# Performance work log

Measured on AMD Instinct MI355X. Metric: run time of the kernel, lower is better.

The kernel has to match this reference:

```python
import jax, jax.numpy as jnp
import numpy as np

B, IN_DIM, H, L, P = 256, 64, 768, 4, 8
EPS = 1e-5


def _layernorm(h, g, b):
    mu = jnp.mean(h, axis=-1, keepdims=True)
    var = jnp.mean((h - mu) ** 2, axis=-1, keepdims=True)
    return (h - mu) * jax.lax.rsqrt(var + EPS) * g + b


def setup_inputs() -> dict:
    key = jax.random.key(0)
    ks = jax.random.split(key, 20)
    s_in = 1.0 / np.sqrt(IN_DIM)
    s_h = 1.0 / np.sqrt(H)
    return {
        "x": jax.random.normal(ks[0], (B, IN_DIM), jnp.float32),
        "w_in": jax.random.normal(ks[1], (IN_DIM, H), jnp.float32) * s_in,
        "b_in": jnp.zeros((H,), jnp.float32),
        "ln_g": jnp.ones((L, H), jnp.float32),
        "ln_b": jnp.zeros((L, H), jnp.float32),
        "trop_w": jax.random.normal(ks[2], (L, H, H), jnp.float32) * s_h,  # [L, out, in]
        "trop_b": jnp.zeros((L, H), jnp.float32),
        "lf_amax": jax.random.normal(ks[3], (L, H, P), jnp.float32) * 0.5 + 1.0,
        "lf_bmax": jax.random.normal(ks[4], (L, H, P), jnp.float32) * 0.1,
        "lf_amin": jax.random.normal(ks[5], (L, H, P), jnp.float32) * 0.5 + 1.0,
        "lf_bmin": jax.random.normal(ks[6], (L, H, P), jnp.float32) * 0.1,
        "lf_alpha": jnp.zeros((L, H), jnp.float32),
        "gate_w": jax.random.normal(ks[7], (L, H, H), jnp.float32) * 0.02,
        "gate_b": jnp.full((L, H), 2.0, jnp.float32),
        "cls_w": jax.random.normal(ks[8], (L, H, H), jnp.float32) * s_h,
        "cls_b": jnp.zeros((L, H), jnp.float32),
        "out_g": jnp.ones((H,), jnp.float32),
        "out_b": jnp.zeros((H,), jnp.float32),
        "head_w": jax.random.normal(ks[9], (H, 1), jnp.float32) * s_h,
        "head_b": jnp.zeros((1,), jnp.float32),
    }


def reference(x, w_in, b_in, ln_g, ln_b, trop_w, trop_b, lf_amax, lf_bmax,
              lf_amin, lf_bmin, lf_alpha, gate_w, gate_b, cls_w, cls_b,
              out_g, out_b, head_w, head_b):
    h = x @ w_in + b_in  # [B, H]
    for l in range(L):
        res = h
        hn = _layernorm(h, ln_g[l], ln_b[l])
        # Tropical (max-plus) linear: y[b,o] = max_i(hn[b,i] + W[o,i]) + bias[o]
        t = jnp.max(hn[:, None, :] + trop_w[l][None, :, :], axis=-1) + trop_b[l]
        # LF dual activation: blend of convex (max-plus) and concave (min-plus) PWL
        fmax = jnp.max(t[..., None] * lf_amax[l] + lf_bmax[l], axis=-1)  # [B, H]
        fmin = jnp.min(t[..., None] * lf_amin[l] + lf_bmin[l], axis=-1)
        a = jax.nn.sigmoid(lf_alpha[l])
        trop_out = a * fmax + (1.0 - a) * fmin
        class_out = jax.nn.gelu(hn @ cls_w[l] + cls_b[l], approximate=False)
        g = jax.nn.sigmoid(hn @ gate_w[l] + gate_b[l])
        h = res + g * trop_out + (1.0 - g) * class_out
    h = _layernorm(h, out_g, out_b)
    return (h @ head_w + head_b).squeeze(-1)  # [B]
```

## Files before the change

kernel.cpp:

```cpp
#include <hip/hip_runtime.h>
#include <math.h>

#define HDIM 768
#define BDIM 256
#define INDIM 64
#define NLAYERS 4
#define PDIM 8
#define KSPLIT 24
#define KLEN 32
#define CHK 16
#define TR 128
#define TC 64
#define NTROPBLK 576
#define NCGBLK 192
#define NBLK (NTROPBLK + NCGBLK)

typedef short bf16x8 __attribute__((ext_vector_type(8)));
typedef float f32x4 __attribute__((ext_vector_type(4)));

__device__ __forceinline__ float sigmoidf_(float x) { return 1.f / (1.f + expf(-x)); }
__device__ __forceinline__ float geluf_(float x) { return 0.5f * x * (1.f + erff(x * 0.70710678118654752f)); }
__device__ __forceinline__ unsigned short f2bf(float f) {
    unsigned int u = __float_as_uint(f);
    u += 0x7FFFu + ((u >> 16) & 1u);
    return (unsigned short)(u >> 16);
}

__device__ __forceinline__ void gload_lds16(const float* g, float* l) {
    __builtin_amdgcn_global_load_lds((const __attribute__((address_space(1))) void*)g,
                                     (__attribute__((address_space(3))) void*)l, 16, 0, 0);
}

__global__ __launch_bounds__(256) void prep_k(const float* __restrict__ trop_w,
                                              const float* __restrict__ cls_w,
                                              const float* __restrict__ gate_w,
                                              float* __restrict__ twT,
                                              unsigned short* __restrict__ wB)
{
    __shared__ float tile[64][65];
    const int z = blockIdx.z;
    const int a0 = blockIdx.x * 64;
    const int b0 = blockIdx.y * 64;
    const int c = threadIdx.x & 63;
    const int r4 = threadIdx.x >> 6;

    if (z < NLAYERS) {
        const float* s = trop_w + (size_t)z * HDIM * HDIM;
        float* d = twT + (size_t)z * HDIM * HDIM;
#pragma unroll
        for (int it = 0; it < 16; ++it) {
            const int r = it * 4 + r4;
            tile[r][c] = s[(size_t)(a0 + r) * HDIM + b0 + c];
        }
        __syncthreads();
#pragma unroll
        for (int it = 0; it < 16; ++it) {
            const int r = it * 4 + r4;
            d[(size_t)(b0 + r) * HDIM + a0 + c] = tile[c][r];
        }
    } else {
        const int zz = z - NLAYERS;
        const int l = zz >> 1, mat = zz & 1;
        const float* s = (mat ? gate_w : cls_w) + (size_t)l * HDIM * HDIM;
        unsigned short* d = wB + (size_t)zz * HDIM * HDIM;
#pragma unroll
        for (int it = 0; it < 16; ++it) {
            const int r = it * 4 + r4;
            tile[r][c] = s[(size_t)(b0 + r) * HDIM + a0 + c];
        }
        __syncthreads();
#pragma unroll
        for (int it = 0; it < 16; ++it) {
            const int r = it * 4 + r4;
            d[(size_t)(a0 + r) * HDIM + b0 + c] = f2bf(tile[c][r]);
        }
    }
}

__global__ __launch_bounds__(256) void input_ln_k(
    const float* __restrict__ x, const float* __restrict__ w_in,
    const float* __restrict__ b_in,
    const float* __restrict__ lng, const float* __restrict__ lnb,
    float* __restrict__ h, float* __restrict__ hnT, unsigned short* __restrict__ hnB)
{
    const int b = blockIdx.x;
    const int t = threadIdx.x;
    __shared__ float xs[INDIM];
    __shared__ float rbuf[8];
    if (t < INDIM) xs[t] = x[b * INDIM + t];
    __syncthreads();

    float acc0 = b_in[t], acc1 = b_in[t + 256], acc2 = b_in[t + 512];
#pragma unroll 8
    for (int i = 0; i < INDIM; ++i) {
        const float xv = xs[i];
        acc0 = fmaf(xv, w_in[i * HDIM + t], acc0);
        acc1 = fmaf(xv, w_in[i * HDIM + t + 256], acc1);
        acc2 = fmaf(xv, w_in[i * HDIM + t + 512], acc2);
    }
    h[(size_t)b * HDIM + t] = acc0;
    h[(size_t)b * HDIM + t + 256] = acc1;
    h[(size_t)b * HDIM + t + 512] = acc2;

    float s = acc0 + acc1 + acc2;
    float q = acc0 * acc0 + acc1 * acc1 + acc2 * acc2;
#pragma unroll
    for (int off = 32; off > 0; off >>= 1) { s += __shfl_down(s, off); q += __shfl_down(q, off); }
    const int wid = t >> 6, lane = t & 63;
    if (lane == 0) { rbuf[wid] = s; rbuf[4 + wid] = q; }
    __syncthreads();
    s = rbuf[0] + rbuf[1] + rbuf[2] + rbuf[3];
    q = rbuf[4] + rbuf[5] + rbuf[6] + rbuf[7];
    const float mu = s * (1.f / HDIM);
    const float var = q * (1.f / HDIM) - mu * mu;
    const float rsig = rsqrtf(var + 1e-5f);

#pragma unroll
    for (int qq = 0; qq < 3; ++qq) {
        const int o = t + qq * 256;
        const float av = (qq == 0) ? acc0 : (qq == 1) ? acc1 : acc2;
        const float v = (av - mu) * rsig * lng[o] + lnb[o];
        hnT[(size_t)o * BDIM + b] = v;
        hnB[(size_t)b * HDIM + o] = f2bf(v);
    }
}

__global__ __launch_bounds__(256, 2) void layer_mm_k(
    const float* __restrict__ hnT,
    const float* __restrict__ twT,
    const unsigned short* __restrict__ hnB,
    const unsigned short* __restrict__ wB,
    float* __restrict__ p_trop, float* __restrict__ p_cls, float* __restrict__ p_gate)
{
    __shared__ float hn_s[2][CHK][TR];
    __shared__ float wt_s[2][CHK][TC];

    const int bx = blockIdx.x;
    const int tid = threadIdx.x;
    const int wave = tid >> 6, lane = tid & 63;

    if (bx < NTROPBLK) {
        const int sp = bx % 24;
        const int slot = bx / 24;
        const int col0 = (sp % 12) * TC;
        const int row0 = (sp / 12) * TR;
        const int k0 = slot * KLEN;

        const int tx = tid & 15, ty = tid >> 4;
        const int r0 = ty * 8, c0 = tx * 4;

        const int hk = lane >> 5;
        const int hcol = (lane & 31) * 4;
        const int wr = lane >> 4;
        const int wcol = (lane & 15) * 4;

        float t_acc[8][4];
#pragma unroll
        for (int i = 0; i < 8; ++i)
#pragma unroll
            for (int j = 0; j < 4; ++j) t_acc[i][j] = -1e30f;

        #define STAGE_T(buf, kb)                                                                   \
        {                                                                                          \
            gload_lds16(hnT + (size_t)((kb) + 4 * wave + hk) * BDIM + row0 + hcol,                 \
                        &hn_s[buf][4 * wave][0]);                                                  \
            gload_lds16(hnT + (size_t)((kb) + 4 * wave + 2 + hk) * BDIM + row0 + hcol,             \
                        &hn_s[buf][4 * wave + 2][0]);                                              \
            gload_lds16(twT + (size_t)((kb) + 4 * wave + wr) * HDIM + col0 + wcol,                 \
                        &wt_s[buf][4 * wave][0]);                                                  \
        }

        STAGE_T(0, k0);
        __builtin_amdgcn_s_waitcnt(0);
        __syncthreads();

        for (int c = 0; c < KLEN / CHK; ++c) {
            const int buf = c & 1;
            if (c + 1 < KLEN / CHK) STAGE_T(1 - buf, k0 + (c + 1) * CHK);
#pragma unroll
            for (int k = 0; k < CHK; ++k) {
                const float4 h0 = *(const float4*)&hn_s[buf][k][r0];
                const float4 h1 = *(const float4*)&hn_s[buf][k][r0 + 4];
                const float4 wt = *(const float4*)&wt_s[buf][k][c0];
                const float hf[8] = {h0.x, h0.y, h0.z, h0.w, h1.x, h1.y, h1.z, h1.w};
                const float wtf[4] = {wt.x, wt.y, wt.z, wt.w};
#pragma unroll
                for (int i = 0; i < 8; ++i)
#pragma unroll
                    for (int j = 0; j < 4; ++j)
                        t_acc[i][j] = fmaxf(t_acc[i][j], hf[i] + wtf[j]);
            }
            __builtin_amdgcn_s_waitcnt(0);
            __syncthreads();
        }
        #undef STAGE_T

        const size_t base = (size_t)slot * BDIM * HDIM;
#pragma unroll
        for (int i = 0; i < 8; ++i) {
            const size_t off = base + (size_t)(row0 + r0 + i) * HDIM + col0 + c0;
            *(float4*)(p_trop + off) = make_float4(t_acc[i][0], t_acc[i][1], t_acc[i][2], t_acc[i][3]);
        }
    } else {
        const int cb = bx - NTROPBLK;
        const int mat = cb & 1;
        const int nt = (cb >> 1) % 24;
        const int mt = cb / 48;
        const int m0 = mt * 64 + wave * 16;
        const int n0 = nt * 32;
        const int lm = lane & 15, q = lane >> 4;

        const unsigned short* wmat = wB + (size_t)mat * HDIM * HDIM;
        float* pout = mat ? p_gate : p_cls;

        f32x4 acc[2];
        acc[0] = (f32x4){0.f, 0.f, 0.f, 0.f};
        acc[1] = (f32x4){0.f, 0.f, 0.f, 0.f};

        const unsigned short* aptr = hnB + (size_t)(m0 + lm) * HDIM + q * 8;
        const unsigned short* b0 = wmat + (size_t)(n0 + lm) * HDIM + q * 8;
        const unsigned short* b1 = b0 + (size_t)16 * HDIM;

#pragma unroll 4
        for (int k0 = 0; k0 < HDIM; k0 += 32) {
            const bf16x8 a  = *(const bf16x8*)(aptr + k0);
            const bf16x8 v0 = *(const bf16x8*)(b0 + k0);
            const bf16x8 v1 = *(const bf16x8*)(b1 + k0);
            acc[0] = __builtin_amdgcn_mfma_f32_16x16x32_bf16(a, v0, acc[0], 0, 0, 0);
            acc[1] = __builtin_amdgcn_mfma_f32_16x16x32_bf16(a, v1, acc[1], 0, 0, 0);
        }

#pragma unroll
        for (int nn = 0; nn < 2; ++nn)
#pragma unroll
            for (int r = 0; r < 4; ++r)
                pout[(size_t)(m0 + q * 4 + r) * HDIM + n0 + nn * 16 + lm] = acc[nn][r];
    }
}

__global__ __launch_bounds__(768) void combine_k(
    const float* __restrict__ p_trop, const float* __restrict__ p_cls, const float* __restrict__ p_gate,
    const float* __restrict__ trop_b,
    const float* __restrict__ amax, const float* __restrict__ bmax,
    const float* __restrict__ amin, const float* __restrict__ bmin,
    const float* __restrict__ alpha,
    const float* __restrict__ gate_b, const float* __restrict__ cls_b,
    float* __restrict__ h,
    const float* __restrict__ lng, const float* __restrict__ lnb,
    float* __restrict__ hnT, unsigned short* __restrict__ hnB,
    const float* __restrict__ head_w, const float* __restrict__ head_b,
    float* __restrict__ out, const int is_last)
{
    const int b = blockIdx.x;
    const int o = threadIdx.x;
    __shared__ float rbuf[12], qbuf[12];

    const size_t base = (size_t)b * HDIM + o;
    float tm = -1e30f;
#pragma unroll
    for (int k = 0; k < KSPLIT; ++k)
        tm = fmaxf(tm, p_trop[(size_t)k * BDIM * HDIM + base]);
    const float cs = p_cls[base];
    const float gs = p_gate[base];

    const float tv = tm + trop_b[o];
    float fmx = -1e30f, fmn = 1e30f;
#pragma unroll
    for (int p = 0; p < PDIM; ++p) {
        fmx = fmaxf(fmx, fmaf(tv, amax[o * PDIM + p], bmax[o * PDIM + p]));
        fmn = fminf(fmn, fmaf(tv, amin[o * PDIM + p], bmin[o * PDIM + p]));
    }
    const float a = sigmoidf_(alpha[o]);
    const float trop_out = a * fmx + (1.f - a) * fmn;
    const float cls_out = geluf_(cs + cls_b[o]);
    const float g = sigmoidf_(gs + gate_b[o]);
    const float val = h[base] + g * trop_out + (1.f - g) * cls_out;
    h[base] = val;

    float s = val, q = val * val;
#pragma unroll
    for (int off = 32; off > 0; off >>= 1) { s += __shfl_down(s, off); q += __shfl_down(q, off); }
    const int wid = o >> 6, lane = o & 63;
    if (lane == 0) { rbuf[wid] = s; qbuf[wid] = q; }
    __syncthreads();
    s = 0.f; q = 0.f;
#pragma unroll
    for (int w = 0; w < 12; ++w) { s += rbuf[w]; q += qbuf[w]; }
    const float mu = s * (1.f / HDIM);
    const float var = q * (1.f / HDIM) - mu * mu;
    const float rsig = rsqrtf(var + 1e-5f);
    const float ln_v = (val - mu) * rsig * lng[o] + lnb[o];

    if (!is_last) {
        hnT[(size_t)o * BDIM + b] = ln_v;
        hnB[base] = f2bf(ln_v);
    } else {
        float part = ln_v * head_w[o];
#pragma unroll
        for (int off = 32; off > 0; off >>= 1) part += __shfl_down(part, off);
        __syncthreads();
        if (lane == 0) rbuf[wid] = part;
        __syncthreads();
        if (o == 0) {
            float r = head_b[0];
#pragma unroll
            for (int w = 0; w < 12; ++w) r += rbuf[w];
            out[b] = r;
        }
    }
}

extern "C" void kernel_launch(void* const* d_in, const int* in_sizes, int n_in,
                              void* d_out, int out_size, void* d_ws, size_t ws_size,
                              hipStream_t stream)
{
    const float* x       = (const float*)d_in[0];
    const float* w_in    = (const float*)d_in[1];
    const float* b_in    = (const float*)d_in[2];
    const float* ln_g    = (const float*)d_in[3];
    const float* ln_b    = (const float*)d_in[4];
    const float* trop_w  = (const float*)d_in[5];
    const float* trop_b  = (const float*)d_in[6];
    const float* lf_amax = (const float*)d_in[7];
    const float* lf_bmax = (const float*)d_in[8];
    const float* lf_amin = (const float*)d_in[9];
    const float* lf_bmin = (const float*)d_in[10];
    const float* lf_alpha= (const float*)d_in[11];
    const float* gate_w  = (const float*)d_in[12];
    const float* gate_b  = (const float*)d_in[13];
    const float* cls_w   = (const float*)d_in[14];
    const float* cls_b   = (const float*)d_in[15];
    const float* out_g   = (const float*)d_in[16];
    const float* out_b   = (const float*)d_in[17];
    const float* head_w  = (const float*)d_in[18];
    const float* head_b  = (const float*)d_in[19];
    float* out = (float*)d_out;

    const size_t NBH = (size_t)BDIM * HDIM;
    const size_t WSZ = (size_t)HDIM * HDIM;
    float* ws = (float*)d_ws;
    float* h      = ws;
    float* hnT    = ws + NBH;
    float* twT    = ws + 2 * NBH;
    float* p_trop = twT + (size_t)NLAYERS * WSZ;
    float* p_cls  = p_trop + (size_t)KSPLIT * NBH;
    float* p_gate = p_cls + NBH;
    unsigned short* hnB = (unsigned short*)(p_gate + NBH);
    unsigned short* wB  = hnB + NBH;

    prep_k<<<dim3(12, 12, 12), 256, 0, stream>>>(trop_w, cls_w, gate_w, twT, wB);
    input_ln_k<<<BDIM, 256, 0, stream>>>(x, w_in, b_in, ln_g, ln_b, h, hnT, hnB);

    for (int l = 0; l < NLAYERS; ++l) {
        layer_mm_k<<<NBLK, 256, 0, stream>>>(
            hnT, twT + (size_t)l * WSZ,
            hnB, wB + (size_t)(2 * l) * WSZ,
            p_trop, p_cls, p_gate);

        const int is_last = (l == NLAYERS - 1);
        combine_k<<<BDIM, 768, 0, stream>>>(
            p_trop, p_cls, p_gate,
            trop_b + (size_t)l * HDIM,
            lf_amax + (size_t)l * HDIM * PDIM, lf_bmax + (size_t)l * HDIM * PDIM,
            lf_amin + (size_t)l * HDIM * PDIM, lf_bmin + (size_t)l * HDIM * PDIM,
            lf_alpha + (size_t)l * HDIM,
            gate_b + (size_t)l * HDIM, cls_b + (size_t)l * HDIM,
            h,
            is_last ? out_g : ln_g + (size_t)(l + 1) * HDIM,
            is_last ? out_b : ln_b + (size_t)(l + 1) * HDIM,
            hnT, hnB, head_w, head_b, out, is_last);
    }
}
```

Baseline: 218.4 us.

## Fuse input, per-layer matmuls and combine into one cooperative persistent kernel

Replaces the input LN kernel and the eight per-layer matmul/combine launches with a single cooperative kernel of 256 workgroups × 768 threads. Each workgroup runs three 256-thread teams for the matmul phases, and grid.sync separates the phases. The tropical K chunk is halved to fit three teams' LDS buffers. This removes launch gaps and tail effects between the nine kernels, at the cost of grid-wide barrier overhead and a fixed grid that may not map as well to the CUs.

```diff
diff --git a/kernel.cpp b/kernel.cpp
--- a/kernel.cpp
+++ b/kernel.cpp
@@ -1,5 +1,8 @@
 #include <hip/hip_runtime.h>
+#include <hip/hip_cooperative_groups.h>
 #include <math.h>
+
+namespace cg = cooperative_groups;
 
 #define HDIM 768
 #define BDIM 256
@@ -8,12 +11,12 @@
 #define PDIM 8
 #define KSPLIT 24
 #define KLEN 32
-#define CHK 16
+#define CHK 8
 #define TR 128
 #define TC 64
-#define NTROPBLK 576
-#define NCGBLK 192
-#define NBLK (NTROPBLK + NCGBLK)
+#define NWG 256
+#define NTHR 768
+#define TROPBLK 192
 
 typedef short bf16x8 __attribute__((ext_vector_type(8)));
 typedef float f32x4 __attribute__((ext_vector_type(4)));
@@ -77,236 +80,229 @@
     }
 }
 
-__global__ __launch_bounds__(256) void input_ln_k(
-    const float* __restrict__ x, const float* __restrict__ w_in,
-    const float* __restrict__ b_in,
-    const float* __restrict__ lng, const float* __restrict__ lnb,
-    float* __restrict__ h, float* __restrict__ hnT, unsigned short* __restrict__ hnB)
-{
-    const int b = blockIdx.x;
-    const int t = threadIdx.x;
-    __shared__ float xs[INDIM];
-    __shared__ float rbuf[8];
-    if (t < INDIM) xs[t] = x[b * INDIM + t];
-    __syncthreads();
-
-    float acc0 = b_in[t], acc1 = b_in[t + 256], acc2 = b_in[t + 512];
-#pragma unroll 8
-    for (int i = 0; i < INDIM; ++i) {
-        const float xv = xs[i];
-        acc0 = fmaf(xv, w_in[i * HDIM + t], acc0);
-        acc1 = fmaf(xv, w_in[i * HDIM + t + 256], acc1);
-        acc2 = fmaf(xv, w_in[i * HDIM + t + 512], acc2);
-    }
-    h[(size_t)b * HDIM + t] = acc0;
-    h[(size_t)b * HDIM + t + 256] = acc1;
-    h[(size_t)b * HDIM + t + 512] = acc2;
-
-    float s = acc0 + acc1 + acc2;
-    float q = acc0 * acc0 + acc1 * acc1 + acc2 * acc2;
-#pragma unroll
-    for (int off = 32; off > 0; off >>= 1) { s += __shfl_down(s, off); q += __shfl_down(q, off); }
-    const int wid = t >> 6, lane = t & 63;
-    if (lane == 0) { rbuf[wid] = s; rbuf[4 + wid] = q; }
-    __syncthreads();
-    s = rbuf[0] + rbuf[1] + rbuf[2] + rbuf[3];
-    q = rbuf[4] + rbuf[5] + rbuf[6] + rbuf[7];
-    const float mu = s * (1.f / HDIM);
-    const float var = q * (1.f / HDIM) - mu * mu;
-    const float rsig = rsqrtf(var + 1e-5f);
-
-#pragma unroll
-    for (int qq = 0; qq < 3; ++qq) {
-        const int o = t + qq * 256;
-        const float av = (qq == 0) ? acc0 : (qq == 1) ? acc1 : acc2;
-        const float v = (av - mu) * rsig * lng[o] + lnb[o];
-        hnT[(size_t)o * BDIM + b] = v;
-        hnB[(size_t)b * HDIM + o] = f2bf(v);
-    }
-}
-
-__global__ __launch_bounds__(256, 2) void layer_mm_k(
-    const float* __restrict__ hnT,
-    const float* __restrict__ twT,
-    const unsigned short* __restrict__ hnB,
-    const unsigned short* __restrict__ wB,
-    float* __restrict__ p_trop, float* __restrict__ p_cls, float* __restrict__ p_gate)
-{
-    __shared__ float hn_s[2][CHK][TR];
-    __shared__ float wt_s[2][CHK][TC];
-
-    const int bx = blockIdx.x;
-    const int tid = threadIdx.x;
-    const int wave = tid >> 6, lane = tid & 63;
-
-    if (bx < NTROPBLK) {
-        const int sp = bx % 24;
-        const int slot = bx / 24;
-        const int col0 = (sp % 12) * TC;
-        const int row0 = (sp / 12) * TR;
-        const int k0 = slot * KLEN;
-
-        const int tx = tid & 15, ty = tid >> 4;
-        const int r0 = ty * 8, c0 = tx * 4;
-
-        const int hk = lane >> 5;
-        const int hcol = (lane & 31) * 4;
-        const int wr = lane >> 4;
-        const int wcol = (lane & 15) * 4;
-
-        float t_acc[8][4];
-#pragma unroll
-        for (int i = 0; i < 8; ++i)
-#pragma unroll
-            for (int j = 0; j < 4; ++j) t_acc[i][j] = -1e30f;
-
-        #define STAGE_T(buf, kb)                                                                   \
-        {                                                                                          \
-            gload_lds16(hnT + (size_t)((kb) + 4 * wave + hk) * BDIM + row0 + hcol,                 \
-                        &hn_s[buf][4 * wave][0]);                                                  \
-            gload_lds16(hnT + (size_t)((kb) + 4 * wave + 2 + hk) * BDIM + row0 + hcol,             \
-                        &hn_s[buf][4 * wave + 2][0]);                                              \
-            gload_lds16(twT + (size_t)((kb) + 4 * wave + wr) * HDIM + col0 + wcol,                 \
-                        &wt_s[buf][4 * wave][0]);                                                  \
-        }
-
-        STAGE_T(0, k0);
-        __builtin_amdgcn_s_waitcnt(0);
-        __syncthreads();
-
-        for (int c = 0; c < KLEN / CHK; ++c) {
-            const int buf = c & 1;
-            if (c + 1 < KLEN / CHK) STAGE_T(1 - buf, k0 + (c + 1) * CHK);
-#pragma unroll
-            for (int k = 0; k < CHK; ++k) {
-                const float4 h0 = *(const float4*)&hn_s[buf][k][r0];
-                const float4 h1 = *(const float4*)&hn_s[buf][k][r0 + 4];
-                const float4 wt = *(const float4*)&wt_s[buf][k][c0];
-                const float hf[8] = {h0.x, h0.y, h0.z, h0.w, h1.x, h1.y, h1.z, h1.w};
-                const float wtf[4] = {wt.x, wt.y, wt.z, wt.w};
-#pragma unroll
-                for (int i = 0; i < 8; ++i)
-#pragma unroll
-                    for (int j = 0; j < 4; ++j)
-                        t_acc[i][j] = fmaxf(t_acc[i][j], hf[i] + wtf[j]);
-            }
-            __builtin_amdgcn_s_waitcnt(0);
-            __syncthreads();
-        }
-        #undef STAGE_T
-
-        const size_t base = (size_t)slot * BDIM * HDIM;
-#pragma unroll
-        for (int i = 0; i < 8; ++i) {
-            const size_t off = base + (size_t)(row0 + r0 + i) * HDIM + col0 + c0;
-            *(float4*)(p_trop + off) = make_float4(t_acc[i][0], t_acc[i][1], t_acc[i][2], t_acc[i][3]);
-        }
-    } else {
-        const int cb = bx - NTROPBLK;
-        const int mat = cb & 1;
-        const int nt = (cb >> 1) % 24;
-        const int mt = cb / 48;
-        const int m0 = mt * 64 + wave * 16;
-        const int n0 = nt * 32;
-        const int lm = lane & 15, q = lane >> 4;
-
-        const unsigned short* wmat = wB + (size_t)mat * HDIM * HDIM;
-        float* pout = mat ? p_gate : p_cls;
-
-        f32x4 acc[2];
-        acc[0] = (f32x4){0.f, 0.f, 0.f, 0.f};
-        acc[1] = (f32x4){0.f, 0.f, 0.f, 0.f};
-
-        const unsigned short* aptr = hnB + (size_t)(m0 + lm) * HDIM + q * 8;
-        const unsigned short* b0 = wmat + (size_t)(n0 + lm) * HDIM + q * 8;
-        const unsigned short* b1 = b0 + (size_t)16 * HDIM;
-
-#pragma unroll 4
-        for (int k0 = 0; k0 < HDIM; k0 += 32) {
-            const bf16x8 a  = *(const bf16x8*)(aptr + k0);
-            const bf16x8 v0 = *(const bf16x8*)(b0 + k0);
-            const bf16x8 v1 = *(const bf16x8*)(b1 + k0);
-            acc[0] = __builtin_amdgcn_mfma_f32_16x16x32_bf16(a, v0, acc[0], 0, 0, 0);
-            acc[1] = __builtin_amdgcn_mfma_f32_16x16x32_bf16(a, v1, acc[1], 0, 0, 0);
-        }
-
-#pragma unroll
-        for (int nn = 0; nn < 2; ++nn)
-#pragma unroll
-            for (int r = 0; r < 4; ++r)
-                pout[(size_t)(m0 + q * 4 + r) * HDIM + n0 + nn * 16 + lm] = acc[nn][r];
-    }
-}
-
-__global__ __launch_bounds__(768) void combine_k(
-    const float* __restrict__ p_trop, const float* __restrict__ p_cls, const float* __restrict__ p_gate,
-    const float* __restrict__ trop_b,
+union SMemU {
+    struct { float hn[3][2][CHK][TR]; float wt[3][2][CHK][TC]; } mm;
+    struct { float xs[INDIM]; float rbuf[12]; float qbuf[12]; } red;
+};
+
+__global__ __launch_bounds__(NTHR, 3) void mega_k(
+    const float* __restrict__ x, const float* __restrict__ w_in, const float* __restrict__ b_in,
+    const float* __restrict__ ln_g, const float* __restrict__ ln_b,
+    const float* __restrict__ twT, const float* __restrict__ trop_b,
     const float* __restrict__ amax, const float* __restrict__ bmax,
     const float* __restrict__ amin, const float* __restrict__ bmin,
     const float* __restrict__ alpha,
     const float* __restrict__ gate_b, const float* __restrict__ cls_b,
-    float* __restrict__ h,
-    const float* __restrict__ lng, const float* __restrict__ lnb,
-    float* __restrict__ hnT, unsigned short* __restrict__ hnB,
+    const unsigned short* __restrict__ wB,
+    const float* __restrict__ out_g, const float* __restrict__ out_b,
     const float* __restrict__ head_w, const float* __restrict__ head_b,
-    float* __restrict__ out, const int is_last)
+    float* __restrict__ h, float* __restrict__ hnT, unsigned short* __restrict__ hnB,
+    float* __restrict__ p_trop, float* __restrict__ p_cls, float* __restrict__ p_gate,
+    float* __restrict__ out)
 {
-    const int b = blockIdx.x;
-    const int o = threadIdx.x;
-    __shared__ float rbuf[12], qbuf[12];
-
-    const size_t base = (size_t)b * HDIM + o;
-    float tm = -1e30f;
-#pragma unroll
-    for (int k = 0; k < KSPLIT; ++k)
-        tm = fmaxf(tm, p_trop[(size_t)k * BDIM * HDIM + base]);
-    const float cs = p_cls[base];
-    const float gs = p_gate[base];
-
-    const float tv = tm + trop_b[o];
-    float fmx = -1e30f, fmn = 1e30f;
-#pragma unroll
-    for (int p = 0; p < PDIM; ++p) {
-        fmx = fmaxf(fmx, fmaf(tv, amax[o * PDIM + p], bmax[o * PDIM + p]));
-        fmn = fminf(fmn, fmaf(tv, amin[o * PDIM + p], bmin[o * PDIM + p]));
+    __shared__ SMemU sm;
+    cg::grid_group grid = cg::this_grid();
+
+    const int bx = blockIdx.x;
+    const int tid = threadIdx.x;
+    const int team = tid >> 8;
+    const int ttid = tid & 255;
+    const int wave = ttid >> 6;
+    const int lane = tid & 63;
+    const size_t NBH = (size_t)BDIM * HDIM;
+    const size_t WSZ = (size_t)HDIM * HDIM;
+
+    {
+        const int b = bx;
+        const int o = tid;
+        if (tid < INDIM) sm.red.xs[tid] = x[b * INDIM + tid];
+        __syncthreads();
+        float acc = b_in[o];
+#pragma unroll 16
+        for (int i = 0; i < INDIM; ++i)
+            acc = fmaf(sm.red.xs[i], w_in[(size_t)i * HDIM + o], acc);
+        h[(size_t)b * HDIM + o] = acc;
+
+        float s = acc, q = acc * acc;
+#pragma unroll
+        for (int off = 32; off > 0; off >>= 1) { s += __shfl_down(s, off); q += __shfl_down(q, off); }
+        const int wid = tid >> 6;
+        if (lane == 0) { sm.red.rbuf[wid] = s; sm.red.qbuf[wid] = q; }
+        __syncthreads();
+        s = 0.f; q = 0.f;
+#pragma unroll
+        for (int w = 0; w < 12; ++w) { s += sm.red.rbuf[w]; q += sm.red.qbuf[w]; }
+        const float mu = s * (1.f / HDIM);
+        const float var = q * (1.f / HDIM) - mu * mu;
+        const float rsig = rsqrtf(var + 1e-5f);
+        const float v = (acc - mu) * rsig * ln_g[o] + ln_b[o];
+        hnT[(size_t)o * BDIM + b] = v;
+        hnB[(size_t)b * HDIM + o] = f2bf(v);
     }
-    const float a = sigmoidf_(alpha[o]);
-    const float trop_out = a * fmx + (1.f - a) * fmn;
-    const float cls_out = geluf_(cs + cls_b[o]);
-    const float g = sigmoidf_(gs + gate_b[o]);
-    const float val = h[base] + g * trop_out + (1.f - g) * cls_out;
-    h[base] = val;
-
-    float s = val, q = val * val;
-#pragma unroll
-    for (int off = 32; off > 0; off >>= 1) { s += __shfl_down(s, off); q += __shfl_down(q, off); }
-    const int wid = o >> 6, lane = o & 63;
-    if (lane == 0) { rbuf[wid] = s; qbuf[wid] = q; }
-    __syncthreads();
-    s = 0.f; q = 0.f;
-#pragma unroll
-    for (int w = 0; w < 12; ++w) { s += rbuf[w]; q += qbuf[w]; }
-    const float mu = s * (1.f / HDIM);
-    const float var = q * (1.f / HDIM) - mu * mu;
-    const float rsig = rsqrtf(var + 1e-5f);
-    const float ln_v = (val - mu) * rsig * lng[o] + lnb[o];
-
-    if (!is_last) {
-        hnT[(size_t)o * BDIM + b] = ln_v;
-        hnB[base] = f2bf(ln_v);
-    } else {
-        float part = ln_v * head_w[o];
-#pragma unroll
-        for (int off = 32; off > 0; off >>= 1) part += __shfl_down(part, off);
-        __syncthreads();
-        if (lane == 0) rbuf[wid] = part;
-        __syncthreads();
-        if (o == 0) {
-            float r = head_b[0];
-#pragma unroll
-            for (int w = 0; w < 12; ++w) r += rbuf[w];
-            out[b] = r;
-        }
+    grid.sync();
+
+    for (int l = 0; l < NLAYERS; ++l) {
+        if (bx < TROPBLK) {
+            const int u = bx * 3 + team;
+            const int sp = u % 24;
+            const int slot = u / 24;
+            const int col0 = (sp % 12) * TC;
+            const int row0 = (sp / 12) * TR;
+            const int k0 = slot * KLEN;
+            const float* twT_l = twT + (size_t)l * WSZ;
+
+            const int tx = ttid & 15, ty = ttid >> 4;
+            const int r0 = ty * 8, c0 = tx * 4;
+            const int hk = lane >> 5, hcol = (lane & 31) * 4;
+            const int wr = lane >> 4, wcol = (lane & 15) * 4;
+
+            float (*hn_s)[CHK][TR] = sm.mm.hn[team];
+            float (*wt_s)[CHK][TC] = sm.mm.wt[team];
+
+            float t_acc[8][4];
+#pragma unroll
+            for (int i = 0; i < 8; ++i)
+#pragma unroll
+                for (int j = 0; j < 4; ++j) t_acc[i][j] = -1e30f;
+
+            #define STAGE_T(bufi, kb)                                                              \
+            {                                                                                      \
+                gload_lds16(hnT + (size_t)((kb) + 2 * wave + hk) * BDIM + row0 + hcol,             \
+                            &hn_s[bufi][2 * wave][0]);                                             \
+                if (wave < 2)                                                                      \
+                    gload_lds16(twT_l + (size_t)((kb) + 4 * wave + wr) * HDIM + col0 + wcol,       \
+                                &wt_s[bufi][4 * wave][0]);                                         \
+            }
+
+            STAGE_T(0, k0);
+            __builtin_amdgcn_s_waitcnt(0);
+            __syncthreads();
+
+            for (int c = 0; c < KLEN / CHK; ++c) {
+                const int buf = c & 1;
+                if (c + 1 < KLEN / CHK) STAGE_T(1 - buf, k0 + (c + 1) * CHK);
+#pragma unroll
+                for (int k = 0; k < CHK; ++k) {
+                    const float4 h0 = *(const float4*)&hn_s[buf][k][r0];
+                    const float4 h1 = *(const float4*)&hn_s[buf][k][r0 + 4];
+                    const float4 w4 = *(const float4*)&wt_s[buf][k][c0];
+                    const float hf[8] = {h0.x, h0.y, h0.z, h0.w, h1.x, h1.y, h1.z, h1.w};
+                    const float wf[4] = {w4.x, w4.y, w4.z, w4.w};
+#pragma unroll
+                    for (int i = 0; i < 8; ++i)
+#pragma unroll
+                        for (int j = 0; j < 4; ++j)
+                            t_acc[i][j] = fmaxf(t_acc[i][j], hf[i] + wf[j]);
+                }
+                __builtin_amdgcn_s_waitcnt(0);
+                __syncthreads();
+            }
+            #undef STAGE_T
+
+            const size_t pb = (size_t)slot * NBH;
+#pragma unroll
+            for (int i = 0; i < 8; ++i) {
+                *(float4*)(p_trop + pb + (size_t)(row0 + r0 + i) * HDIM + col0 + c0) =
+                    make_float4(t_acc[i][0], t_acc[i][1], t_acc[i][2], t_acc[i][3]);
+            }
+        } else {
+            const int u = (bx - TROPBLK) * 3 + team;
+            const int mat = u & 1;
+            const int nt = (u >> 1) % 24;
+            const int mt = u / 48;
+            const int m0 = mt * 64 + wave * 16;
+            const int n0 = nt * 32;
+            const int lm = lane & 15, qq = lane >> 4;
+
+            const unsigned short* wmat = wB + (size_t)(2 * l + mat) * WSZ;
+            float* pout = mat ? p_gate : p_cls;
+
+            f32x4 acc0 = (f32x4){0.f, 0.f, 0.f, 0.f};
+            f32x4 acc1 = (f32x4){0.f, 0.f, 0.f, 0.f};
+
+            const unsigned short* aptr = hnB + (size_t)(m0 + lm) * HDIM + qq * 8;
+            const unsigned short* bp0 = wmat + (size_t)(n0 + lm) * HDIM + qq * 8;
+            const unsigned short* bp1 = bp0 + (size_t)16 * HDIM;
+
+#pragma unroll 4
+            for (int kk = 0; kk < HDIM; kk += 32) {
+                const bf16x8 a  = *(const bf16x8*)(aptr + kk);
+                const bf16x8 v0 = *(const bf16x8*)(bp0 + kk);
+                const bf16x8 v1 = *(const bf16x8*)(bp1 + kk);
+                acc0 = __builtin_amdgcn_mfma_f32_16x16x32_bf16(a, v0, acc0, 0, 0, 0);
+                acc1 = __builtin_amdgcn_mfma_f32_16x16x32_bf16(a, v1, acc1, 0, 0, 0);
+            }
+#pragma unroll
+            for (int r = 0; r < 4; ++r) {
+                pout[(size_t)(m0 + qq * 4 + r) * HDIM + n0 + lm] = acc0[r];
+                pout[(size_t)(m0 + qq * 4 + r) * HDIM + n0 + 16 + lm] = acc1[r];
+            }
+        }
+        grid.sync();
+
+        {
+            const int b = bx;
+            const int o = tid;
+            const int is_last = (l == NLAYERS - 1);
+
+            const size_t base = (size_t)b * HDIM + o;
+            float tm = -1e30f;
+#pragma unroll
+            for (int k = 0; k < KSPLIT; ++k)
+                tm = fmaxf(tm, p_trop[(size_t)k * NBH + base]);
+            const float cs = p_cls[base];
+            const float gs = p_gate[base];
+
+            const float tv = tm + trop_b[(size_t)l * HDIM + o];
+            float fmx = -1e30f, fmn = 1e30f;
+            const size_t po = ((size_t)l * HDIM + o) * PDIM;
+#pragma unroll
+            for (int p = 0; p < PDIM; ++p) {
+                fmx = fmaxf(fmx, fmaf(tv, amax[po + p], bmax[po + p]));
+                fmn = fminf(fmn, fmaf(tv, amin[po + p], bmin[po + p]));
+            }
+            const float a = sigmoidf_(alpha[(size_t)l * HDIM + o]);
+            const float trop_out = a * fmx + (1.f - a) * fmn;
+            const float cls_out = geluf_(cs + cls_b[(size_t)l * HDIM + o]);
+            const float g = sigmoidf_(gs + gate_b[(size_t)l * HDIM + o]);
+            const float val = h[base] + g * trop_out + (1.f - g) * cls_out;
+            h[base] = val;
+
+            float s = val, q = val * val;
+#pragma unroll
+            for (int off = 32; off > 0; off >>= 1) { s += __shfl_down(s, off); q += __shfl_down(q, off); }
+            const int wid = o >> 6;
+            if (lane == 0) { sm.red.rbuf[wid] = s; sm.red.qbuf[wid] = q; }
+            __syncthreads();
+            s = 0.f; q = 0.f;
+#pragma unroll
+            for (int w = 0; w < 12; ++w) { s += sm.red.rbuf[w]; q += sm.red.qbuf[w]; }
+            const float mu = s * (1.f / HDIM);
+            const float var = q * (1.f / HDIM) - mu * mu;
+            const float rsig = rsqrtf(var + 1e-5f);
+            const float* lngp = is_last ? out_g : ln_g + (size_t)(l + 1) * HDIM;
+            const float* lnbp = is_last ? out_b : ln_b + (size_t)(l + 1) * HDIM;
+            const float ln_v = (val - mu) * rsig * lngp[o] + lnbp[o];
+
+            if (!is_last) {
+                hnT[(size_t)o * BDIM + b] = ln_v;
+                hnB[base] = f2bf(ln_v);
+            } else {
+                float part = ln_v * head_w[o];
+#pragma unroll
+                for (int off = 32; off > 0; off >>= 1) part += __shfl_down(part, off);
+                __syncthreads();
+                if (lane == 0) sm.red.rbuf[wid] = part;
+                __syncthreads();
+                if (o == 0) {
+                    float r = head_b[0];
+#pragma unroll
+                    for (int w = 0; w < 12; ++w) r += sm.red.rbuf[w];
+                    out[b] = r;
+                }
+            }
+        }
+        if (l != NLAYERS - 1) grid.sync();
     }
 }
 
@@ -349,25 +345,15 @@
     unsigned short* wB  = hnB + NBH;
 
     prep_k<<<dim3(12, 12, 12), 256, 0, stream>>>(trop_w, cls_w, gate_w, twT, wB);
-    input_ln_k<<<BDIM, 256, 0, stream>>>(x, w_in, b_in, ln_g, ln_b, h, hnT, hnB);
-
-    for (int l = 0; l < NLAYERS; ++l) {
-        layer_mm_k<<<NBLK, 256, 0, stream>>>(
-            hnT, twT + (size_t)l * WSZ,
-            hnB, wB + (size_t)(2 * l) * WSZ,
-            p_trop, p_cls, p_gate);
-
-        const int is_last = (l == NLAYERS - 1);
-        combine_k<<<BDIM, 768, 0, stream>>>(
-            p_trop, p_cls, p_gate,
-            trop_b + (size_t)l * HDIM,
-            lf_amax + (size_t)l * HDIM * PDIM, lf_bmax + (size_t)l * HDIM * PDIM,
-            lf_amin + (size_t)l * HDIM * PDIM, lf_bmin + (size_t)l * HDIM * PDIM,
-            lf_alpha + (size_t)l * HDIM,
-            gate_b + (size_t)l * HDIM, cls_b + (size_t)l * HDIM,
-            h,
-            is_last ? out_g : ln_g + (size_t)(l + 1) * HDIM,
-            is_last ? out_b : ln_b + (size_t)(l + 1) * HDIM,
-            hnT, hnB, head_w, head_b, out, is_last);
-    }
-}
+
+    void* args[] = {
+        (void*)&x, (void*)&w_in, (void*)&b_in, (void*)&ln_g, (void*)&ln_b,
+        (void*)&twT, (void*)&trop_b,
+        (void*)&lf_amax, (void*)&lf_bmax, (void*)&lf_amin, (void*)&lf_bmin,
+        (void*)&lf_alpha, (void*)&gate_b, (void*)&cls_b,
+        (void*)&wB, (void*)&out_g, (void*)&out_b, (void*)&head_w, (void*)&head_b,
+        (void*)&h, (void*)&hnT, (void*)&hnB,
+        (void*)&p_trop, (void*)&p_cls, (void*)&p_gate, (void*)&out
+    };
+    hipLaunchCooperativeKernel((void*)mega_k, dim3(NWG), dim3(NTHR), args, 0, stream);
+}
```

Result: slower. 525.7 us (+140.8%).

## Fuse input LN into prep kernel, single-stage tropical tile, interleave block types

Applied to the files above, without the earlier changes.

The input projection plus LayerNorm is folded into the weight-prep kernel as extra z-slices, removing one launch. The tropical max-plus tile now loads its whole 32-deep K chunk into LDS at once instead of double-buffering two 16-deep chunks, dropping one barrier round. Tropical and MFMA blocks are interleaved three-to-one across the grid so both kinds are spread over the CUs. The partial-result stride is padded to an odd-ish value (PSTRIDE) to reduce channel or cache aliasing between split-K slices. LDS use per block stays the same and there is no longer any load/compute overlap inside the tropical path.

```diff
diff --git a/kernel.cpp b/kernel.cpp
--- a/kernel.cpp
+++ b/kernel.cpp
@@ -8,12 +8,10 @@
 #define PDIM 8
 #define KSPLIT 24
 #define KLEN 32
-#define CHK 16
 #define TR 128
 #define TC 64
-#define NTROPBLK 576
-#define NCGBLK 192
-#define NBLK (NTROPBLK + NCGBLK)
+#define NBLK 768
+#define PSTRIDE 196864
 
 typedef short bf16x8 __attribute__((ext_vector_type(8)));
 typedef float f32x4 __attribute__((ext_vector_type(4)));
@@ -35,7 +33,15 @@
                                               const float* __restrict__ cls_w,
                                               const float* __restrict__ gate_w,
                                               float* __restrict__ twT,
-                                              unsigned short* __restrict__ wB)
+                                              unsigned short* __restrict__ wB,
+                                              const float* __restrict__ x,
+                                              const float* __restrict__ w_in,
+                                              const float* __restrict__ b_in,
+                                              const float* __restrict__ lng,
+                                              const float* __restrict__ lnb,
+                                              float* __restrict__ h,
+                                              float* __restrict__ hnT,
+                                              unsigned short* __restrict__ hnB)
 {
     __shared__ float tile[64][65];
     const int z = blockIdx.z;
@@ -58,7 +64,7 @@
             const int r = it * 4 + r4;
             d[(size_t)(b0 + r) * HDIM + a0 + c] = tile[c][r];
         }
-    } else {
+    } else if (z < 12) {
         const int zz = z - NLAYERS;
         const int l = zz >> 1, mat = zz & 1;
         const float* s = (mat ? gate_w : cls_w) + (size_t)l * HDIM * HDIM;
@@ -74,74 +80,71 @@
             const int r = it * 4 + r4;
             d[(size_t)(a0 + r) * HDIM + b0 + c] = f2bf(tile[c][r]);
         }
-    }
-}
-
-__global__ __launch_bounds__(256) void input_ln_k(
-    const float* __restrict__ x, const float* __restrict__ w_in,
-    const float* __restrict__ b_in,
-    const float* __restrict__ lng, const float* __restrict__ lnb,
-    float* __restrict__ h, float* __restrict__ hnT, unsigned short* __restrict__ hnB)
-{
-    const int b = blockIdx.x;
-    const int t = threadIdx.x;
-    __shared__ float xs[INDIM];
-    __shared__ float rbuf[8];
-    if (t < INDIM) xs[t] = x[b * INDIM + t];
-    __syncthreads();
-
-    float acc0 = b_in[t], acc1 = b_in[t + 256], acc2 = b_in[t + 512];
+    } else {
+        const int idx = (z - 12) * 144 + blockIdx.y * 12 + blockIdx.x;
+        if (idx >= BDIM) return;
+        const int b = idx;
+        const int t = threadIdx.x;
+        float* xs = &tile[0][0];
+        float* rb = &tile[1][0];
+        if (t < INDIM) xs[t] = x[b * INDIM + t];
+        __syncthreads();
+
+        float acc0 = b_in[t], acc1 = b_in[t + 256], acc2 = b_in[t + 512];
 #pragma unroll 8
-    for (int i = 0; i < INDIM; ++i) {
-        const float xv = xs[i];
-        acc0 = fmaf(xv, w_in[i * HDIM + t], acc0);
-        acc1 = fmaf(xv, w_in[i * HDIM + t + 256], acc1);
-        acc2 = fmaf(xv, w_in[i * HDIM + t + 512], acc2);
-    }
-    h[(size_t)b * HDIM + t] = acc0;
-    h[(size_t)b * HDIM + t + 256] = acc1;
-    h[(size_t)b * HDIM + t + 512] = acc2;
-
-    float s = acc0 + acc1 + acc2;
-    float q = acc0 * acc0 + acc1 * acc1 + acc2 * acc2;
-#pragma unroll
-    for (int off = 32; off > 0; off >>= 1) { s += __shfl_down(s, off); q += __shfl_down(q, off); }
-    const int wid = t >> 6, lane = t & 63;
-    if (lane == 0) { rbuf[wid] = s; rbuf[4 + wid] = q; }
-    __syncthreads();
-    s = rbuf[0] + rbuf[1] + rbuf[2] + rbuf[3];
-    q = rbuf[4] + rbuf[5] + rbuf[6] + rbuf[7];
-    const float mu = s * (1.f / HDIM);
-    const float var = q * (1.f / HDIM) - mu * mu;
-    const float rsig = rsqrtf(var + 1e-5f);
-
-#pragma unroll
-    for (int qq = 0; qq < 3; ++qq) {
-        const int o = t + qq * 256;
-        const float av = (qq == 0) ? acc0 : (qq == 1) ? acc1 : acc2;
-        const float v = (av - mu) * rsig * lng[o] + lnb[o];
-        hnT[(size_t)o * BDIM + b] = v;
-        hnB[(size_t)b * HDIM + o] = f2bf(v);
+        for (int i = 0; i < INDIM; ++i) {
+            const float xv = xs[i];
+            acc0 = fmaf(xv, w_in[(size_t)i * HDIM + t], acc0);
+            acc1 = fmaf(xv, w_in[(size_t)i * HDIM + t + 256], acc1);
+            acc2 = fmaf(xv, w_in[(size_t)i * HDIM + t + 512], acc2);
+        }
+        h[(size_t)b * HDIM + t] = acc0;
+        h[(size_t)b * HDIM + t + 256] = acc1;
+        h[(size_t)b * HDIM + t + 512] = acc2;
+
+        float s = acc0 + acc1 + acc2;
+        float q = acc0 * acc0 + acc1 * acc1 + acc2 * acc2;
+#pragma unroll
+        for (int off = 32; off > 0; off >>= 1) { s += __shfl_down(s, off); q += __shfl_down(q, off); }
+        const int wid = t >> 6, lane = t & 63;
+        if (lane == 0) { rb[wid] = s; rb[4 + wid] = q; }
+        __syncthreads();
+        s = rb[0] + rb[1] + rb[2] + rb[3];
+        q = rb[4] + rb[5] + rb[6] + rb[7];
+        const float mu = s * (1.f / HDIM);
+        const float var = q * (1.f / HDIM) - mu * mu;
+        const float rsig = rsqrtf(var + 1e-5f);
+
+#pragma unroll
+        for (int qq = 0; qq < 3; ++qq) {
+            const int o = t + qq * 256;
+            const float av = (qq == 0) ? acc0 : (qq == 1) ? acc1 : acc2;
+            const float v = (av - mu) * rsig * lng[o] + lnb[o];
+            hnT[(size_t)o * BDIM + b] = v;
+            hnB[(size_t)b * HDIM + o] = f2bf(v);
+        }
     }
 }
 
 __global__ __launch_bounds__(256, 2) void layer_mm_k(
     const float* __restrict__ hnT,
-    const float* __restrict__ twT,
+    const float* __restrict__ twT_l,
     const unsigned short* __restrict__ hnB,
-    const unsigned short* __restrict__ wB,
+    const unsigned short* __restrict__ wB_l,
     float* __restrict__ p_trop, float* __restrict__ p_cls, float* __restrict__ p_gate)
 {
-    __shared__ float hn_s[2][CHK][TR];
-    __shared__ float wt_s[2][CHK][TC];
+    __shared__ float hn_s[KLEN][TR];
+    __shared__ float wt_s[KLEN][TC];
 
     const int bx = blockIdx.x;
     const int tid = threadIdx.x;
     const int wave = tid >> 6, lane = tid & 63;
-
-    if (bx < NTROPBLK) {
-        const int sp = bx % 24;
-        const int slot = bx / 24;
+    const int rblk = bx & 3, qblk = bx >> 2;
+
+    if (rblk < 3) {
+        const int u = qblk * 3 + rblk;
+        const int sp = u % 24;
+        const int slot = u / 24;
         const int col0 = (sp % 12) * TC;
         const int row0 = (sp / 12) * TR;
         const int k0 = slot * KLEN;
@@ -154,55 +157,46 @@
         const int wr = lane >> 4;
         const int wcol = (lane & 15) * 4;
 
+#pragma unroll
+        for (int i = 0; i < 4; ++i)
+            gload_lds16(hnT + (size_t)(k0 + 8 * wave + 2 * i + hk) * BDIM + row0 + hcol,
+                        &hn_s[8 * wave + 2 * i][0]);
+#pragma unroll
+        for (int i = 0; i < 2; ++i)
+            gload_lds16(twT_l + (size_t)(k0 + 8 * wave + 4 * i + wr) * HDIM + col0 + wcol,
+                        &wt_s[8 * wave + 4 * i][0]);
+
         float t_acc[8][4];
 #pragma unroll
         for (int i = 0; i < 8; ++i)
 #pragma unroll
             for (int j = 0; j < 4; ++j) t_acc[i][j] = -1e30f;
 
-        #define STAGE_T(buf, kb)                                                                   \
-        {                                                                                          \
-            gload_lds16(hnT + (size_t)((kb) + 4 * wave + hk) * BDIM + row0 + hcol,                 \
-                        &hn_s[buf][4 * wave][0]);                                                  \
-            gload_lds16(hnT + (size_t)((kb) + 4 * wave + 2 + hk) * BDIM + row0 + hcol,             \
-                        &hn_s[buf][4 * wave + 2][0]);                                              \
-            gload_lds16(twT + (size_t)((kb) + 4 * wave + wr) * HDIM + col0 + wcol,                 \
-                        &wt_s[buf][4 * wave][0]);                                                  \
-        }
-
-        STAGE_T(0, k0);
         __builtin_amdgcn_s_waitcnt(0);
         __syncthreads();
 
-        for (int c = 0; c < KLEN / CHK; ++c) {
-            const int buf = c & 1;
-            if (c + 1 < KLEN / CHK) STAGE_T(1 - buf, k0 + (c + 1) * CHK);
-#pragma unroll
-            for (int k = 0; k < CHK; ++k) {
-                const float4 h0 = *(const float4*)&hn_s[buf][k][r0];
-                const float4 h1 = *(const float4*)&hn_s[buf][k][r0 + 4];
-                const float4 wt = *(const float4*)&wt_s[buf][k][c0];
-                const float hf[8] = {h0.x, h0.y, h0.z, h0.w, h1.x, h1.y, h1.z, h1.w};
-                const float wtf[4] = {wt.x, wt.y, wt.z, wt.w};
-#pragma unroll
-                for (int i = 0; i < 8; ++i)
-#pragma unroll
-                    for (int j = 0; j < 4; ++j)
-                        t_acc[i][j] = fmaxf(t_acc[i][j], hf[i] + wtf[j]);
-            }
-            __builtin_amdgcn_s_waitcnt(0);
-            __syncthreads();
-        }
-        #undef STAGE_T
-
-        const size_t base = (size_t)slot * BDIM * HDIM;
+#pragma unroll 16
+        for (int k = 0; k < KLEN; ++k) {
+            const float4 h0 = *(const float4*)&hn_s[k][r0];
+            const float4 h1 = *(const float4*)&hn_s[k][r0 + 4];
+            const float4 wt = *(const float4*)&wt_s[k][c0];
+            const float hf[8] = {h0.x, h0.y, h0.z, h0.w, h1.x, h1.y, h1.z, h1.w};
+            const float wtf[4] = {wt.x, wt.y, wt.z, wt.w};
+#pragma unroll
+            for (int i = 0; i < 8; ++i)
+#pragma unroll
+                for (int j = 0; j < 4; ++j)
+                    t_acc[i][j] = fmaxf(t_acc[i][j], hf[i] + wtf[j]);
+        }
+
+        const size_t base = (size_t)slot * PSTRIDE;
 #pragma unroll
         for (int i = 0; i < 8; ++i) {
             const size_t off = base + (size_t)(row0 + r0 + i) * HDIM + col0 + c0;
             *(float4*)(p_trop + off) = make_float4(t_acc[i][0], t_acc[i][1], t_acc[i][2], t_acc[i][3]);
         }
     } else {
-        const int cb = bx - NTROPBLK;
+        const int cb = qblk;
         const int mat = cb & 1;
         const int nt = (cb >> 1) % 24;
         const int mt = cb / 48;
@@ -210,7 +204,7 @@
         const int n0 = nt * 32;
         const int lm = lane & 15, q = lane >> 4;
 
-        const unsigned short* wmat = wB + (size_t)mat * HDIM * HDIM;
+        const unsigned short* wmat = wB_l + (size_t)mat * HDIM * HDIM;
         float* pout = mat ? p_gate : p_cls;
 
         f32x4 acc[2];
@@ -259,7 +253,7 @@
     float tm = -1e30f;
 #pragma unroll
     for (int k = 0; k < KSPLIT; ++k)
-        tm = fmaxf(tm, p_trop[(size_t)k * BDIM * HDIM + base]);
+        tm = fmaxf(tm, p_trop[(size_t)k * PSTRIDE + base]);
     const float cs = p_cls[base];
     const float gs = p_gate[base];
 
@@ -343,13 +337,14 @@
     float* hnT    = ws + NBH;
     float* twT    = ws + 2 * NBH;
     float* p_trop = twT + (size_t)NLAYERS * WSZ;
-    float* p_cls  = p_trop + (size_t)KSPLIT * NBH;
+    float* p_cls  = p_trop + (size_t)KSPLIT * PSTRIDE;
     float* p_gate = p_cls + NBH;
     unsigned short* hnB = (unsigned short*)(p_gate + NBH);
     unsigned short* wB  = hnB + NBH;
 
-    prep_k<<<dim3(12, 12, 12), 256, 0, stream>>>(trop_w, cls_w, gate_w, twT, wB);
-    input_ln_k<<<BDIM, 256, 0, stream>>>(x, w_in, b_in, ln_g, ln_b, h, hnT, hnB);
+    prep_k<<<dim3(12, 12, 14), 256, 0, stream>>>(trop_w, cls_w, gate_w, twT, wB,
+                                                 x, w_in, b_in, ln_g, ln_b,
+                                                 h, hnT, hnB);
 
     for (int l = 0; l < NLAYERS; ++l) {
         layer_mm_k<<<NBLK, 256, 0, stream>>>(
```

Result: slower. 258.4 us (+18.3%).
